# Kernel tuning notes

Measured on AMD Instinct MI355X. Metric: run time of the kernel, lower is better.

The kernel has to match this reference:

```python
import jax, jax.numpy as jnp
import numpy as np

STRIDE = 8
NUM_POINTS = 17
OFFSET_RANGE = 1.5
NUM_HEADS = 4
BASE_OFFSETS = np.array([(-1,-1),(-1,0),(-1,1),(0,-1),(0,0),(0,1),(1,-1),(1,0),(1,1),
                         (-3,-3),(-3,0),(-3,3),(0,-3),(0,3),(3,-3),(3,0),(3,3)], dtype=np.float32)


def setup_inputs() -> dict:
    key = jax.random.key(0)
    ks = jax.random.split(key, 16)
    N, D, P, B = 40000, 128, NUM_POINTS, 2
    Hf, Wf, H_img, W_img = 56, 100, 448, 800
    x_lidar = jax.random.normal(ks[0], (N, D), jnp.float32)
    b_idx = jax.random.randint(ks[1], (N, 1), 0, B)
    z = jax.random.randint(ks[2], (N, 1), 0, 10)
    y = jax.random.randint(ks[3], (N, 1), 0, 125)
    x = jax.random.randint(ks[4], (N, 1), 0, 125)
    indices = jnp.concatenate([b_idx, z, y, x], axis=1).astype(jnp.int32)
    img_feats = jax.random.normal(ks[5], (B, D, Hf, Wf), jnp.float32)
    voxel_size = jnp.array([0.1, 0.1, 0.1], jnp.float32)
    pc_range = jnp.array([-50.0, -50.0, -5.0, 50.0, 50.0, 3.0], jnp.float32)
    # plausible lidar->image projection: intrinsics @ extrinsics (x-forward -> z-forward)
    K = np.array([[600.0, 0.0, W_img / 2.0], [0.0, 600.0, H_img / 2.0], [0.0, 0.0, 1.0]])
    Rt = np.array([[0.0, -1.0, 0.0, 0.0], [0.0, 0.0, -1.0, 1.5], [1.0, 0.0, 0.0, 0.0]])
    P34 = (K @ Rt).astype(np.float32)
    trans_lidar_to_img = jnp.asarray(np.stack([P34, P34]))
    s = 0.02
    return {
        'x_lidar': x_lidar,
        'indices': indices,
        'img_feats': img_feats,
        'voxel_size': voxel_size,
        'pc_range': pc_range,
        'trans_lidar_to_img': trans_lidar_to_img,
        'offset_W': jax.random.normal(ks[6], (D, 2 * P), jnp.float32) * s,
        'offset_b': jax.random.normal(ks[7], (2 * P,), jnp.float32) * s,
        'q_W': jax.random.normal(ks[8], (D, D), jnp.float32) * s,
        'q_b': jnp.zeros((D,), jnp.float32),
        'k_W': jax.random.normal(ks[9], (D, D), jnp.float32) * s,
        'k_b': jnp.zeros((D,), jnp.float32),
        'v_W': jax.random.normal(ks[10], (D, D), jnp.float32) * s,
        'v_b': jnp.zeros((D,), jnp.float32),
        'out_W': jax.random.normal(ks[11], (D, D), jnp.float32) * s,
        'out_b': jnp.zeros((D,), jnp.float32),
        'H_img': H_img,
        'W_img': W_img,
    }


def _forward(x_lidar, indices, img_feats, voxel_size, pc_range, trans_lidar_to_img,
             offset_W, offset_b, q_W, q_b, k_W, k_b, v_W, v_b, out_W, out_b, H_img, W_img):
    N, D = x_lidar.shape
    B, C, Hf, Wf = img_feats.shape
    bidx = indices[:, 0].astype(jnp.int32)
    # --- project voxel centers to normalized image coords ---
    spatial = indices[:, jnp.array([3, 2, 1])].astype(jnp.float32)  # (x, y, z) order
    cvs = voxel_size * STRIDE
    phys = spatial * cvs + pc_range[:3] + cvs * 0.5                 # [N,3]
    hom = jnp.concatenate([phys, jnp.ones((N, 1), phys.dtype)], axis=1)
    pts = jnp.einsum('nij,nj->ni', trans_lidar_to_img[bidx], hom)   # [N,3]
    depth = jnp.maximum(pts[:, 2], 1e-5)
    u_feat = (pts[:, 0] / depth) * (float(Wf) / float(W_img))
    v_feat = (pts[:, 1] / depth) * (float(Hf) / float(H_img))
    u_n = 2.0 * (u_feat / max(Wf - 1, 1)) - 1.0
    v_n = 2.0 * (v_feat / max(Hf - 1, 1)) - 1.0
    centers = jnp.stack([u_n, v_n], axis=-1)                        # [N,2]
    # --- sampling grid: base ring + learned tanh offsets ---
    du = 2.0 / max(Wf - 1, 1)
    dv = 2.0 / max(Hf - 1, 1)
    base = jnp.asarray(BASE_OFFSETS) * jnp.array([du, dv], jnp.float32)  # [P,2]
    learned = jnp.tanh(x_lidar @ offset_W + offset_b).reshape(N, NUM_POINTS, 2)
    learned = learned * jnp.array([OFFSET_RANGE * du, OFFSET_RANGE * dv], jnp.float32)
    grid = centers[:, None, :] + base[None] + learned               # [N,P,2]
    gx, gy = grid[..., 0], grid[..., 1]
    valid = (jnp.abs(gx) <= 1.0) & (jnp.abs(gy) <= 1.0)             # [N,P]
    # --- bilinear grid_sample, align_corners=True, zeros padding, batched gather ---
    px = (gx + 1.0) * 0.5 * (Wf - 1)
    py = (gy + 1.0) * 0.5 * (Hf - 1)
    x0 = jnp.floor(px).astype(jnp.int32)
    y0 = jnp.floor(py).astype(jnp.int32)
    fx = px - x0
    fy = py - y0
    sampled = jnp.zeros((N, NUM_POINTS, C), x_lidar.dtype)
    for dx_, wx in ((0, 1.0 - fx), (1, fx)):
        for dy_, wy in ((0, 1.0 - fy), (1, fy)):
            xc = x0 + dx_
            yc = y0 + dy_
            inb = (xc >= 0) & (xc < Wf) & (yc >= 0) & (yc < Hf)
            w = wx * wy * inb
            val = img_feats[bidx[:, None], :, jnp.clip(yc, 0, Hf - 1), jnp.clip(xc, 0, Wf - 1)]  # [N,P,C]
            sampled = sampled + val * w[..., None]
    # --- single-query cross attention over sampled points ---
    scale = float(D // NUM_HEADS) ** -0.5
    q = x_lidar @ q_W + q_b                                         # [N,D]
    k = sampled @ k_W + k_b                                         # [N,P,D]
    v = sampled @ v_W + v_b
    attn = jnp.einsum('nd,npd->np', q, k) * scale
    attn = jnp.where(valid, attn, -10000.0)
    attn = jax.nn.softmax(attn, axis=-1)
    attn = attn * valid
    attn = attn / jnp.maximum(attn.sum(-1, keepdims=True), 1e-6)
    out = jnp.einsum('np,npd->nd', attn, v)
    out = out @ out_W + out_b
    # --- rectifier stats ---
    offset_scale = OFFSET_RANGE * max((du ** 2 + dv ** 2) ** 0.5, 1e-6)
    instability = jnp.linalg.norm(learned, axis=-1).mean(-1, keepdims=True) / offset_scale
    offset_stability = jnp.clip(jnp.exp(-instability), 0.0, 1.0)
    valid_sample_ratio = valid.astype(jnp.float32).mean(-1, keepdims=True)
    p = jnp.clip(attn, 1e-6, None)
    entropy = -(p * jnp.log(p)).sum(-1, keepdims=True)
    attn_focus = jnp.clip(1.0 - entropy / float(np.log(max(NUM_POINTS, 2))), 0.0, 1.0)
    return out, valid_sample_ratio, offset_stability, attn_focus


def reference(x_lidar, indices, img_feats, voxel_size, pc_range, trans_lidar_to_img,
              offset_W, offset_b, q_W, q_b, k_W, k_b, v_W, v_b, out_W, out_b, H_img, W_img):
    return _forward(x_lidar, indices, img_feats, voxel_size, pc_range, trans_lidar_to_img,
                    offset_W, offset_b, q_W, q_b, k_W, k_b, v_W, v_b, out_W, out_b, H_img, W_img)
```

## Files before the change

kernel.cpp:

```cpp
#include <hip/hip_runtime.h>
#include <hip/hip_fp16.h>
#include <math.h>

#define NPTS 17
#define DCH 128
#define HF 56
#define WF 100

using half8 = __attribute__((ext_vector_type(8))) _Float16;
using f32x4 = __attribute__((ext_vector_type(4))) float;

#define OFF_WKB    0
#define OFF_A0     128
#define OFF_B0     256
#define OFF_C0     384
#define OFF_W2T    512
#define OFF_BMT    8704
#define OFF_WOFS   16896
#define OFF_FEAT   23040
#define OFF_UVB    739840
#define OFF_IDX    899840
#define OFF_CNT    939840

__device__ inline __half2 bc_h2(unsigned u) { return __builtin_bit_cast(__half2, u); }
__device__ inline unsigned bc_u32(__half2 h) { return __builtin_bit_cast(unsigned, h); }
__device__ inline unsigned packh2(float a, float b) {
  return bc_u32(__float22half2_rn(make_float2(a, b)));
}
__device__ inline ushort f2hu(float x) {
  __half h = __float2half(x);
  return __builtin_bit_cast(ushort, h);
}

__device__ inline int swz(int row, int bcol) {
  return (row << 8) + (bcol ^ ((row & 7) << 4));
}
__device__ inline int swz7(int row, int bcol) {
  return (row << 7) + (bcol ^ ((row & 7) << 4));
}

__device__ inline void project(int4 iv, const float* voxel_size,
    const float* pc_range, const float* trans, float winv, float hinv,
    float& u_n, float& v_n, int& bidx)
{
  bidx = iv.x;
  float cv0 = voxel_size[0]*8.f, cv1 = voxel_size[1]*8.f, cv2 = voxel_size[2]*8.f;
  float ph0 = (float)iv.w*cv0 + pc_range[0] + 0.5f*cv0;
  float ph1 = (float)iv.z*cv1 + pc_range[1] + 0.5f*cv1;
  float ph2 = (float)iv.y*cv2 + pc_range[2] + 0.5f*cv2;
  const float* T = trans + bidx*12;
  float p0 = T[0]*ph0 + T[1]*ph1 + T[2]*ph2  + T[3];
  float p1 = T[4]*ph0 + T[5]*ph1 + T[6]*ph2  + T[7];
  float p2 = T[8]*ph0 + T[9]*ph1 + T[10]*ph2 + T[11];
  float depth = fmaxf(p2, 1e-5f);
  u_n = 2.f*((p0/depth)*winv/99.f) - 1.f;
  v_n = 2.f*((p1/depth)*hinv/55.f) - 1.f;
}

__global__ __launch_bounds__(256) void prep_kernel(
    const float* __restrict__ img,
    const float* __restrict__ q_W, const float* __restrict__ k_W,
    const float* __restrict__ v_W, const float* __restrict__ out_W,
    const float* __restrict__ q_b, const float* __restrict__ k_b,
    const float* __restrict__ v_b,
    const float* __restrict__ offset_W,
    const int* __restrict__ indices,
    const float* __restrict__ voxel_size, const float* __restrict__ pc_range,
    const float* __restrict__ trans,
    const int* __restrict__ HimgP, const int* __restrict__ WimgP,
    float* __restrict__ ws, int N, int nbc)
{
  __shared__ __align__(16) char smraw[32768];
  int tid = threadIdx.x;
  int bid = blockIdx.x;

  if (bid < 448) {
    float* sm = (float*)smraw;
    int by = bid >> 2, q = bid & 3;
    int b = by / HF, y = by % HF;
    const float* src = img + (size_t)b*DCH*HF*WF + (size_t)q*32*HF*WF + y*WF;
    #pragma unroll
    for (int i = 0; i < 13; ++i) {
      int flat = i*256 + tid;
      if (flat < 3200) {
        int c = flat / WF;
        int x = flat - c*WF;
        sm[c*101 + x] = src[(size_t)c*HF*WF + x];
      }
    }
    __syncthreads();
    unsigned* dst = (unsigned*)((ushort*)(ws + OFF_FEAT) + (size_t)(b*HF*WF + y*WF)*DCH);
    #pragma unroll
    for (int i = 0; i < 7; ++i) {
      int flat = i*256 + tid;
      if (flat < 1600) {
        int x = flat >> 4;
        int cp = flat & 15;
        dst[(size_t)x*64 + q*16 + cp] = packh2(sm[(2*cp)*101 + x], sm[(2*cp+1)*101 + x]);
      }
    }
    return;
  }
  bid -= 448;

  if (bid < nbc) {
    int* lc = (int*)smraw;
    int lane = tid & 63;
    unsigned long long lmlt = (1ull << lane) - 1ull;
    const float du = 2.0f/99.0f, dv = 2.0f/55.0f;
    float winv = (float)WF / (float)(WimgP[0]);
    float hinv = (float)HF / (float)(HimgP[0]);
    if (tid < 2) lc[tid] = 0;
    __syncthreads();
    int myslot[4];
    bool inA[4], skipA[4];
    #pragma unroll
    for (int j = 0; j < 4; ++j) {
      int n = bid*1024 + j*256 + tid;
      bool in = (n < N);
      bool cskip = true;
      if (in) {
        float u_n, v_n; int bx;
        project(((const int4*)indices)[n], voxel_size, pc_range, trans, winv, hinv,
                u_n, v_n, bx);
        cskip = (fabsf(u_n) > 1.001f + 4.5f*du) || (fabsf(v_n) > 1.001f + 4.5f*dv);
        if (!cskip)
          ((float4*)(ws + OFF_UVB))[n] = make_float4(u_n, v_n, (float)bx, 0.f);
      }
      inA[j] = in; skipA[j] = cskip;
      unsigned long long mv = __ballot(in && !cskip);
      unsigned long long ms = __ballot(in && cskip);
      int wv = 0, wsk = 0;
      if (lane == 0) {
        wv  = atomicAdd(&lc[0], (int)__popcll(mv));
        wsk = atomicAdd(&lc[1], (int)__popcll(ms));
      }
      wv  = __shfl(wv, 0);
      wsk = __shfl(wsk, 0);
      myslot[j] = cskip ? (wsk + (int)__popcll(ms & lmlt))
                        : (wv  + (int)__popcll(mv & lmlt));
    }
    __syncthreads();
    if (tid == 0) {
      unsigned long long pk = (unsigned long long)(unsigned)lc[0]
                            | ((unsigned long long)(unsigned)lc[1] << 32);
      unsigned long long old = atomicAdd((unsigned long long*)(ws + OFF_CNT), pk);
      lc[2] = (int)(unsigned)old;
      lc[3] = (int)(unsigned)(old >> 32);
    }
    __syncthreads();
    int* idx = (int*)(ws + OFF_IDX);
    #pragma unroll
    for (int j = 0; j < 4; ++j) {
      int n = bid*1024 + j*256 + tid;
      if (inA[j]) {
        if (!skipA[j]) idx[lc[2] + myslot[j]] = n;
        else           idx[N - 1 - (lc[3] + myslot[j])] = n;
      }
    }
    return;
  }
  bid -= nbc;

  if (bid == 0) {
    char* Als = smraw;
    char* Bls = smraw + 16384;
    ushort* w2t = (ushort*)(ws + OFF_W2T);
    int wid = tid >> 6, l = tid & 63, lr = l & 15, lg = l >> 4;
    f32x4 acc[2][8] = {};
    for (int ko = 0; ko < 2; ++ko) {
      __syncthreads();
      #pragma unroll
      for (int i = 0; i < 16; ++i) {
        int flat = i*256 + tid;
        int r = flat >> 5, kp = flat & 31;
        float2 va = *(const float2*)&k_W[r*DCH + ko*64 + 2*kp];
        float2 vb = *(const float2*)&q_W[r*DCH + ko*64 + 2*kp];
        *(unsigned*)(Als + swz7(r, kp*4)) = packh2(va.x, va.y);
        *(unsigned*)(Bls + swz7(r, kp*4)) = packh2(vb.x, vb.y);
      }
      __syncthreads();
      #pragma unroll
      for (int kc = 0; kc < 2; ++kc) {
        int kb = kc*64 + lg*16;
        half8 a0 = *(const half8*)(Als + swz7(wid*32 + lr, kb));
        half8 a1 = *(const half8*)(Als + swz7(wid*32 + 16 + lr, kb));
        #pragma unroll
        for (int ni = 0; ni < 8; ++ni) {
          half8 b = *(const half8*)(Bls + swz7(ni*16 + lr, kb));
          acc[0][ni] = __builtin_amdgcn_mfma_f32_16x16x32_f16(a0, b, acc[0][ni], 0, 0, 0);
          acc[1][ni] = __builtin_amdgcn_mfma_f32_16x16x32_f16(a1, b, acc[1][ni], 0, 0, 0);
        }
      }
    }
    #pragma unroll
    for (int mi = 0; mi < 2; ++mi)
      #pragma unroll
      for (int reg = 0; reg < 4; ++reg) {
        int n = wid*32 + mi*16 + lg*4 + reg;
        #pragma unroll
        for (int ni = 0; ni < 8; ++ni)
          w2t[n*DCH + ni*16 + lr] = f2hu(acc[mi][ni][reg]);
      }
    return;
  }
  bid -= 1;

  if (bid == 0) {
    char* Als = smraw;
    char* Bls = smraw + 16384;
    ushort* bmt = (ushort*)(ws + OFF_BMT);
    int wid = tid >> 6, l = tid & 63, lr = l & 15, lg = l >> 4;
    f32x4 acc[2][8] = {};
    for (int ko = 0; ko < 2; ++ko) {
      __syncthreads();
// ... 45 lines not shown
    __syncthreads();
    int r = tid & 127;
    const float* M  = (tid < 128) ? k_W : q_W;
    const float* vv = (tid < 128) ? vbs : vbs + 128;
    float acc = 0.f;
    #pragma unroll 8
    for (int e = 0; e < DCH; e += 4) {
      float4 m = *(const float4*)&M[(size_t)r*DCH + e];
      acc += m.x*vv[e] + m.y*vv[e+1] + m.z*vv[e+2] + m.w*vv[e+3];
    }
    ws[((tid < 128) ? OFF_A0 : OFF_WKB) + r] = acc;
    if (tid < 128) {
      float b0 = 0.f;
      #pragma unroll 8
      for (int e = 0; e < DCH; ++e) b0 += vbs[256 + e] * out_W[(size_t)e*DCH + tid];
      ws[OFF_B0 + tid] = b0;
    }
    if (tid < 64) {
      float c = vbs[tid]*vbs[128+tid] + vbs[64+tid]*vbs[192+tid];
      c += __shfl_xor(c, 32); c += __shfl_xor(c, 16); c += __shfl_xor(c, 8);
      c += __shfl_xor(c, 4);  c += __shfl_xor(c, 2);  c += __shfl_xor(c, 1);
      if (tid == 0) ws[OFF_C0] = c;
    }
    ushort* woh = (ushort*)(ws + OFF_WOFS);
    ushort* wol = woh + 48*128;
    #pragma unroll
    for (int i = 0; i < 24; ++i) {
      int flat = i*256 + tid;
      int c = flat >> 7, k = flat & 127;
      float wv = (c < 34) ? offset_W[(size_t)k*34 + c] : 0.f;
      __half hw = __float2half(wv);
      woh[flat] = __builtin_bit_cast(ushort, hw);
      wol[flat] = f2hu(wv - __half2float(hw));
    }
  }
}

__device__ inline void fill_point(float* out, const float* out_b,
                                  float instab, int pt, int mm, int N)
{
  const float du = 2.0f/99.0f, dv = 2.0f/55.0f;
  *(float4*)&out[(size_t)pt*DCH + 8*mm]     = *(const float4*)&out_b[8*mm];
  *(float4*)&out[(size_t)pt*DCH + 8*mm + 4] = *(const float4*)&out_b[8*mm + 4];
  if (mm == 0) {
    out[(size_t)N*128 + pt] = 0.f;
    float osc = 1.5f * sqrtf(du*du + dv*dv);
    float inst = (instab / 17.f) / fmaxf(osc, 1e-6f);
    out[(size_t)N*129 + pt] = fminf(fmaxf(__expf(-inst), 0.f), 1.f);
    float ent = 17.f * 1.3815511e-5f;
    out[(size_t)N*130 + pt] = fminf(fmaxf(1.f - ent / logf(17.f), 0.f), 1.f);
  }
}

__global__ __launch_bounds__(256) void fuse_kernel(
    const float* __restrict__ X,
    const float* __restrict__ offset_b,
    const float* __restrict__ out_b,
    float* __restrict__ ws, float* __restrict__ out, int N)
{
  __shared__ __align__(16) char B_lds[32768];
  __shared__ __align__(16) char A_lds[4096];
  __shared__ __align__(16) char Q_lds[4096];
  __shared__ float lrn_lds[16][36];
  __shared__ float sa_lds[16];

  int tid  = threadIdx.x;
  int wave = tid >> 6, lane = tid & 63;
  int g = lane >> 4, mm = lane & 15;
  int lr = lane & 15, lg = lane >> 4;
  int n0 = blockIdx.x * 16;
  int nvalid = ((const int*)(ws + OFF_CNT))[0];
  const int* idxp = (const int*)(ws + OFF_IDX);
  int slot = n0 + wave*4 + g;
  int row  = wave*4 + g;

  {
    int r  = tid >> 4;
    int k0 = (tid & 15) * 8;
    int sl = n0 + r; if (sl >= N) sl = N - 1;
    int pr = idxp[sl];
    const float* xp = &X[(size_t)pr*DCH + k0];
    float4 v0 = *(const float4*)xp;
    float4 v1 = *(const float4*)(xp + 4);
    __half h0 = __float2half(v0.x), h1 = __float2half(v0.y);
    __half h2 = __float2half(v0.z), h3 = __float2half(v0.w);
    __half h4 = __float2half(v1.x), h5 = __float2half(v1.y);
    __half h6 = __float2half(v1.z), h7 = __float2half(v1.w);
    uint4 hw;
    hw.x = bc_u32(__halves2half2(h0, h1)); hw.y = bc_u32(__halves2half2(h2, h3));
    hw.z = bc_u32(__halves2half2(h4, h5)); hw.w = bc_u32(__halves2half2(h6, h7));
    uint4 lw;
    lw.x = packh2(v0.x - __half2float(h0), v0.y - __half2float(h1));
    lw.y = packh2(v0.z - __half2float(h2), v0.w - __half2float(h3));
    lw.z = packh2(v1.x - __half2float(h4), v1.y - __half2float(h5));
    lw.w = packh2(v1.z - __half2float(h6), v1.w - __half2float(h7));
    *(uint4*)(A_lds + swz(r, k0*2)) = hw;
    *(uint4*)(Q_lds + swz(r, k0*2)) = lw;
  }
  {
    const ushort* woh = (const ushort*)(ws + OFF_WOFS);
    const ushort* wol = woh + 48*128;
    #pragma unroll
    for (int i = 0; i < 3; ++i) {
      int flat = i*256 + tid;
      int r = flat >> 4, kq = (flat & 15) * 8;
      *(uint4*)(B_lds + swz(r, kq*2))         = *(const uint4*)&woh[r*128 + kq];
      *(uint4*)(B_lds + 12288 + swz(r, kq*2)) = *(const uint4*)&wol[r*128 + kq];
    }
  }
  __syncthreads();

  const float du = 2.0f/99.0f, dv = 2.0f/55.0f;

  if (wave < 3) {
    f32x4 acc = {};
    #pragma unroll
    for (int kc = 0; kc < 4; ++kc) {
      int kb = kc*64 + lg*16;
      half8 ah = *(const half8*)(A_lds + swz(lr, kb));
      half8 al = *(const half8*)(Q_lds + swz(lr, kb));
      half8 bh = *(const half8*)(B_lds + swz(wave*16 + lr, kb));
      half8 bl = *(const half8*)(B_lds + 12288 + swz(wave*16 + lr, kb));
      acc = __builtin_amdgcn_mfma_f32_16x16x32_f16(al, bh, acc, 0, 0, 0);
      acc = __builtin_amdgcn_mfma_f32_16x16x32_f16(ah, bl, acc, 0, 0, 0);
      acc = __builtin_amdgcn_mfma_f32_16x16x32_f16(ah, bh, acc, 0, 0, 0);
    }
    int o = wave*16 + lr;
    if (o < 34) {
      float sc = (o & 1) ? 1.5f*dv : 1.5f*du;
      float ob = offset_b[o];
      #pragma unroll
      for (int reg = 0; reg < 4; ++reg)
        lrn_lds[lg*4 + reg][o] = tanhf(acc[reg] + ob) * sc;
    }
  }

  float ck;
  {
    uint4 xr = *(const uint4*)(A_lds + swz(row, 16*mm));
    const float* wk = ws + OFF_WKB + 8*mm;
    __half2 x01 = bc_h2(xr.x), x23 = bc_h2(xr.y), x45 = bc_h2(xr.z), x67 = bc_h2(xr.w);
    float s = __low2float(x01)*wk[0] + __high2float(x01)*wk[1]
            + __low2float(x23)*wk[2] + __high2float(x23)*wk[3]
            + __low2float(x45)*wk[4] + __high2float(x45)*wk[5]
            + __low2float(x67)*wk[6] + __high2float(x67)*wk[7];
    s += __shfl_xor(s, 8); s += __shfl_xor(s, 4);
    s += __shfl_xor(s, 2); s += __shfl_xor(s, 1);
    ck = s + ws[OFF_C0];
  }
  __syncthreads();

  float instab;
  {
    float a = lrn_lds[row][2*mm], b = lrn_lds[row][2*mm + 1];
    float s = sqrtf(a*a + b*b);
    if (mm == 0) {
      float a2 = lrn_lds[row][32], b2 = lrn_lds[row][33];
      s += sqrtf(a2*a2 + b2*b2);
    }
    s += __shfl_xor(s, 1); s += __shfl_xor(s, 2);
    s += __shfl_xor(s, 4); s += __shfl_xor(s, 8);
    instab = s;
  }

  if (n0 >= nvalid) {
    if (slot < N) fill_point(out, out_b, instab, idxp[slot], mm, N);
    return;
  }

  {
    const ushort* w2t = (const ushort*)(ws + OFF_W2T);
    #pragma unroll
    for (int i = 0; i < 8; ++i) {
      int flat = i*2048 + tid*8;
      int r = flat >> 7, k = flat & 127;
      *(uint4*)(B_lds + swz(r, k*2)) = *(const uint4*)&w2t[(size_t)r*DCH + k];
    }
  }
  __syncthreads();

  {
    f32x4 qacc[2] = {};
    #pragma unroll
    for (int kc = 0; kc < 4; ++kc) {
      int kb = kc*64 + lg*16;
      half8 a  = *(const half8*)(A_lds + swz(lr, kb));
      half8 b0 = *(const half8*)(B_lds + swz(wave*32 + lr, kb));
      half8 b1 = *(const half8*)(B_lds + swz(wave*32 + 16 + lr, kb));
      qacc[0] = __builtin_amdgcn_mfma_f32_16x16x32_f16(a, b0, qacc[0], 0, 0, 0);
      qacc[1] = __builtin_amdgcn_mfma_f32_16x16x32_f16(a, b1, qacc[1], 0, 0, 0);
    }
    #pragma unroll
    for (int ni = 0; ni < 2; ++ni)
      #pragma unroll
      for (int reg = 0; reg < 4; ++reg) {
        int r = lg*4 + reg;
        int c = wave*32 + ni*16 + lr;
        *(ushort*)(Q_lds + swz(r, c*2)) = f2hu(qacc[ni][reg] + ws[OFF_A0 + c]);
      }
  }
  __syncthreads();

  {
    const ushort* bmt = (const ushort*)(ws + OFF_BMT);
    #pragma unroll
    for (int i = 0; i < 8; ++i) {
      int flat = i*2048 + tid*8;
      int r = flat >> 7, k = flat & 127;
      *(uint4*)(B_lds + swz(r, k*2)) = *(const uint4*)&bmt[(size_t)r*DCH + k];
    }
  }

  if (slot >= nvalid) {
    if (mm == 0) sa_lds[row] = 0.f;
    uint4 z; z.x = 0u; z.y = 0u; z.z = 0u; z.w = 0u;
    *(uint4*)(Q_lds + swz(row, 16*mm)) = z;
    if (slot < N) fill_point(out, out_b, instab, idxp[slot], mm, N);
  } else {
    int pt = idxp[slot];
    float4 uv = ((const float4*)(ws + OFF_UVB))[pt];
    float u_n = uv.x, v_n = uv.y;
    int bidx = (int)uv.z;

    uint4 qp = *(const uint4*)(Q_lds + swz(row, 16*mm));
    __half2 q01 = bc_h2(qp.x), q23 = bc_h2(qp.y), q45 = bc_h2(qp.z), q67 = bc_h2(qp.w);

    const float BOX[NPTS] = {-1,-1,-1, 0,0,0, 1,1,1, -3,-3,-3, 0,0, 3,3,3};
    const float BOY[NPTS] = {-1, 0, 1,-1,0,1,-1,0,1, -3, 0, 3, -3,3,-3,0,3};
    const float scale = 0.17677669529663689f;
    const char* fb = (const char*)(ws + OFF_FEAT);

    float larr[NPTS];
    unsigned vm = 0;
    float m_run = -1e28f, srun = 0.f;
    __half2 pre01 = __float2half2_rn(0.f), pre23 = __float2half2_rn(0.f);
    __half2 pre45 = __float2half2_rn(0.f), pre67 = __float2half2_rn(0.f);
    int fbase = bidx * (HF*WF);
    int moff = mm * 16;

    #pragma unroll
    for (int p = 0; p < NPTS; ++p) {
      float2 lrn = *(const float2*)&lrn_lds[row][2*p];
      float gx = u_n + BOX[p]*du + lrn.x;
      float gy = v_n + BOY[p]*dv + lrn.y;
      bool valid = (fabsf(gx) <= 1.f) && (fabsf(gy) <= 1.f);
      float l = -1e30f;
      if (valid) {
        vm |= (1u << p);
        float px = fmaf(gx, 49.5f, 49.5f);
        float py = fmaf(gy, 27.5f, 27.5f);
        float fpx = floorf(px), fpy = floorf(py);
        float fx = px - fpx, fy = py - fpy;
        int x0 = (int)fpx, y0 = (int)fpy;
        int x1 = min(x0 + 1, WF - 1), y1 = min(y0 + 1, HF - 1);
        float wy0 = 1.f - fy, wx0 = 1.f - fx;
        __half2 h00 = __float2half2_rn(wy0*wx0);
        __half2 h01 = __float2half2_rn(wy0*fx);
        __half2 h10 = __float2half2_rn(fy*wx0);
        __half2 h11 = __float2half2_rn(fy*fx);
        int r0 = (fbase + y0*WF) << 8, r1 = (fbase + y1*WF) << 8;
        uint4 f00 = *(const uint4*)(fb + r0 + (x0 << 8) + moff);
        uint4 f01 = *(const uint4*)(fb + r0 + (x1 << 8) + moff);
        uint4 f10 = *(const uint4*)(fb + r1 + (x0 << 8) + moff);
        uint4 f11 = *(const uint4*)(fb + r1 + (x1 << 8) + moff);
        __half2 s01 = __hfma2(h00, bc_h2(f00.x),
                      __hfma2(h01, bc_h2(f01.x),
                      __hfma2(h10, bc_h2(f10.x),
                      __hmul2(h11, bc_h2(f11.x)))));
        __half2 s23 = __hfma2(h00, bc_h2(f00.y),
                      __hfma2(h01, bc_h2(f01.y),
                      __hfma2(h10, bc_h2(f10.y),
                      __hmul2(h11, bc_h2(f11.y)))));
        __half2 s45 = __hfma2(h00, bc_h2(f00.z),
                      __hfma2(h01, bc_h2(f01.z),
                      __hfma2(h10, bc_h2(f10.z),
                      __hmul2(h11, bc_h2(f11.z)))));
        __half2 s67 = __hfma2(h00, bc_h2(f00.w),
                      __hfma2(h01, bc_h2(f01.w),
                      __hfma2(h10, bc_h2(f10.w),
                      __hmul2(h11, bc_h2(f11.w)))));
        __half2 dh = __hfma2(s01, q01, __hfma2(s23, q23,
                     __hfma2(s45, q45, __hmul2(s67, q67))));
        float part = __low2float(dh) + __high2float(dh);
        part += __shfl_xor(part, 8);
        part += __shfl_xor(part, 4);
        part += __shfl_xor(part, 2);
        part += __shfl_xor(part, 1);
        l = (part + ck) * scale;
        float nm  = fmaxf(m_run, l);
        float esc = __expf(m_run - nm);
        float a   = __expf(l - nm);
        m_run = nm;
        srun = srun*esc + a;
        __half2 esch = __float2half2_rn(esc);
        __half2 ah   = __float2half2_rn(a);
        pre01 = __hfma2(ah, s01, __hmul2(pre01, esch));
        pre23 = __hfma2(ah, s23, __hmul2(pre23, esch));
        pre45 = __hfma2(ah, s45, __hmul2(pre45, esch));
        pre67 = __hfma2(ah, s67, __hmul2(pre67, esch));
      }
      larr[p] = l;
    }

    bool anyv = (vm != 0);
    float offv = anyv ? (m_run + __logf(srun)) : 1e38f;
    float invs = anyv ? 1.f/srun : 0.f;
    __half2 ih = __float2half2_rn(invs);
    pre01 = __hmul2(pre01, ih);
    pre23 = __hmul2(pre23, ih);
    pre45 = __hmul2(pre45, ih);
    pre67 = __hmul2(pre67, ih);

    float ent = 0.f;
    #pragma unroll
    for (int p = 0; p < NPTS; ++p) {
      float d = offv - larr[p];
      float a = __expf(-d);
      ent += (a >= 1e-6f) ? a*d : 1.3815511e-5f;
    }

    uint4 pw;
    pw.x = bc_u32(pre01);
    pw.y = bc_u32(pre23);
    pw.z = bc_u32(pre45);
    pw.w = bc_u32(pre67);
    *(uint4*)(Q_lds + swz(row, 16*mm)) = pw;
    if (mm == 0) {
      sa_lds[row] = anyv ? 1.f : 0.f;
      out[(size_t)N*128 + pt] = (float)__popc(vm) / 17.f;
      float osc = 1.5f * sqrtf(du*du + dv*dv);
      float inst = (instab / 17.f) / fmaxf(osc, 1e-6f);
      out[(size_t)N*129 + pt] = fminf(fmaxf(__expf(-inst), 0.f), 1.f);
      out[(size_t)N*130 + pt] = fminf(fmaxf(1.f - ent / logf(17.f), 0.f), 1.f);
    }
  }
  __syncthreads();

  {
    f32x4 oacc[2] = {};
    #pragma unroll
    for (int kc = 0; kc < 4; ++kc) {
      int kb = kc*64 + lg*16;
      half8 a  = *(const half8*)(Q_lds + swz(lr, kb));
      half8 b0 = *(const half8*)(B_lds + swz(wave*32 + lr, kb));
      half8 b1 = *(const half8*)(B_lds + swz(wave*32 + 16 + lr, kb));
      oacc[0] = __builtin_amdgcn_mfma_f32_16x16x32_f16(a, b0, oacc[0], 0, 0, 0);
      oacc[1] = __builtin_amdgcn_mfma_f32_16x16x32_f16(a, b1, oacc[1], 0, 0, 0);
    }
    #pragma unroll
    for (int reg = 0; reg < 4; ++reg) {
      int r = lg*4 + reg;
      int sl2 = n0 + r;
      if (sl2 >= nvalid) continue;
      int p2 = idxp[sl2];
      float sa = sa_lds[r];
      #pragma unroll
      for (int ni = 0; ni < 2; ++ni) {
        int c = wave*32 + ni*16 + lr;
        out[(size_t)p2*DCH + c] = oacc[ni][reg] + sa*ws[OFF_B0 + c] + out_b[c];
      }
    }
  }
}

extern "C" void kernel_launch(void* const* d_in, const int* in_sizes, int n_in,
                              void* d_out, int out_size, void* d_ws, size_t ws_size,
                              hipStream_t stream) {
  const float* x_lidar    = (const float*)d_in[0];
  const int*   indices    = (const int*)  d_in[1];
  const float* img        = (const float*)d_in[2];
  const float* voxel_size = (const float*)d_in[3];
  const float* pc_range   = (const float*)d_in[4];
  const float* trans      = (const float*)d_in[5];
  const float* offset_W   = (const float*)d_in[6];
  const float* offset_b   = (const float*)d_in[7];
  const float* q_W        = (const float*)d_in[8];
  const float* q_b        = (const float*)d_in[9];
  const float* k_W        = (const float*)d_in[10];
  const float* k_b        = (const float*)d_in[11];
  const float* v_W        = (const float*)d_in[12];
  const float* v_b        = (const float*)d_in[13];
  const float* out_W      = (const float*)d_in[14];
  const float* out_b      = (const float*)d_in[15];
  const int*   Himg       = (const int*)  d_in[16];
  const int*   Wimg       = (const int*)  d_in[17];
  float* ws  = (float*)d_ws;
  float* out = (float*)d_out;
  int N = in_sizes[0] / DCH;
  int nbc = (N + 1023) / 1024;

  hipMemsetAsync(ws + OFF_CNT, 0, 2*sizeof(int), stream);
  hipLaunchKernelGGL(prep_kernel, dim3(448 + nbc + 3), dim3(256), 0, stream,
                     img, q_W, k_W, v_W, out_W, q_b, k_b, v_b,
                     offset_W, indices, voxel_size, pc_range, trans,
                     Himg, Wimg, ws, N, nbc);
  hipLaunchKernelGGL(fuse_kernel, dim3((N + 15) / 16), dim3(256), 0, stream,
                     x_lidar, offset_b, out_b, ws, out, N);
}
```

Baseline: 47.45 us.

## Replace global atomic compaction with per-segment local compaction, drop memset

The valid/skip point compaction now happens separately in each 1024-point segment: each prep block writes its own valid count and index list into its segment region rather than reserving space through a global 64-bit atomic. The fuse kernel grid becomes 64 blocks per segment and reads its segment's count. This removes the hipMemsetAsync call, the global atomic and one block barrier. In exchange, some fuse blocks now mix valid and skipped points or exit at once, so the work per block is less uniform than with one global sorted list.

After: 63.38 us. 1.34x slower.

```diff
diff --git a/kernel.cpp b/kernel.cpp
--- a/kernel.cpp
+++ b/kernel.cpp
@@ -20,7 +20,7 @@
 #define OFF_FEAT   23040
 #define OFF_UVB    739840
 #define OFF_IDX    899840
-#define OFF_CNT    939840
+#define OFF_SCNT   939840
 
 __device__ inline __half2 bc_h2(unsigned u) { return __builtin_bit_cast(__half2, u); }
 __device__ inline unsigned bc_u32(__half2 h) { return __builtin_bit_cast(unsigned, h); }
@@ -68,7 +68,7 @@
     const float* __restrict__ voxel_size, const float* __restrict__ pc_range,
     const float* __restrict__ trans,
     const int* __restrict__ HimgP, const int* __restrict__ WimgP,
-    float* __restrict__ ws, int N, int nbc)
+    float* __restrict__ ws, int N, int nseg)
 {
   __shared__ __align__(16) char smraw[32768];
   int tid = threadIdx.x;
@@ -103,8 +103,11 @@
   }
   bid -= 448;
 
-  if (bid < nbc) {
+  if (bid < nseg) {
     int* lc = (int*)smraw;
+    int seg = bid;
+    int base = seg << 10;
+    int seg_n = N - base; if (seg_n > 1024) seg_n = 1024;
     int lane = tid & 63;
     unsigned long long lmlt = (1ull << lane) - 1ull;
     const float du = 2.0f/99.0f, dv = 2.0f/55.0f;
@@ -116,8 +119,9 @@
     bool inA[4], skipA[4];
     #pragma unroll
     for (int j = 0; j < 4; ++j) {
-      int n = bid*1024 + j*256 + tid;
-      bool in = (n < N);
+      int loc = j*256 + tid;
+      int n = base + loc;
+      bool in = (loc < seg_n);
       bool cskip = true;
       if (in) {
         float u_n, v_n; int bx;
@@ -141,26 +145,19 @@
                         : (wv  + (int)__popcll(mv & lmlt));
     }
     __syncthreads();
-    if (tid == 0) {
-      unsigned long long pk = (unsigned long long)(unsigned)lc[0]
-                            | ((unsigned long long)(unsigned)lc[1] << 32);
-      unsigned long long old = atomicAdd((unsigned long long*)(ws + OFF_CNT), pk);
-      lc[2] = (int)(unsigned)old;
-      lc[3] = (int)(unsigned)(old >> 32);
-    }
-    __syncthreads();
-    int* idx = (int*)(ws + OFF_IDX);
+    if (tid == 0) ((int*)(ws + OFF_SCNT))[seg] = lc[0];
+    int* idx = (int*)(ws + OFF_IDX) + base;
     #pragma unroll
     for (int j = 0; j < 4; ++j) {
-      int n = bid*1024 + j*256 + tid;
+      int n = base + j*256 + tid;
       if (inA[j]) {
-        if (!skipA[j]) idx[lc[2] + myslot[j]] = n;
-        else           idx[N - 1 - (lc[3] + myslot[j])] = n;
+        if (!skipA[j]) idx[myslot[j]] = n;
+        else           idx[seg_n - 1 - myslot[j]] = n;
       }
     }
     return;
   }
-  bid -= nbc;
+  bid -= nseg;
 
   if (bid == 0) {
     char* Als = smraw;
@@ -328,16 +325,21 @@
   int wave = tid >> 6, lane = tid & 63;
   int g = lane >> 4, mm = lane & 15;
   int lr = lane & 15, lg = lane >> 4;
-  int n0 = blockIdx.x * 16;
-  int nvalid = ((const int*)(ws + OFF_CNT))[0];
-  const int* idxp = (const int*)(ws + OFF_IDX);
-  int slot = n0 + wave*4 + g;
+  int seg  = blockIdx.x >> 6;
+  int jblk = blockIdx.x & 63;
+  int base = seg << 10;
+  int seg_n = N - base; if (seg_n > 1024) seg_n = 1024;
+  int n0l = jblk * 16;
+  if (n0l >= seg_n) return;
+  int nvalid = ((const int*)(ws + OFF_SCNT))[seg];
+  const int* idxp = (const int*)(ws + OFF_IDX) + base;
+  int slot = n0l + wave*4 + g;
   int row  = wave*4 + g;
 
   {
     int r  = tid >> 4;
     int k0 = (tid & 15) * 8;
-    int sl = n0 + r; if (sl >= N) sl = N - 1;
+    int sl = n0l + r; if (sl >= seg_n) sl = seg_n - 1;
     int pr = idxp[sl];
     const float* xp = &X[(size_t)pr*DCH + k0];
     float4 v0 = *(const float4*)xp;
@@ -423,8 +425,8 @@
     instab = s;
   }
 
-  if (n0 >= nvalid) {
-    if (slot < N) fill_point(out, out_b, instab, idxp[slot], mm, N);
+  if (n0l >= nvalid) {
+    if (slot < seg_n) fill_point(out, out_b, instab, idxp[slot], mm, N);
     return;
   }
 
@@ -475,7 +477,7 @@
     if (mm == 0) sa_lds[row] = 0.f;
     uint4 z; z.x = 0u; z.y = 0u; z.z = 0u; z.w = 0u;
     *(uint4*)(Q_lds + swz(row, 16*mm)) = z;
-    if (slot < N) fill_point(out, out_b, instab, idxp[slot], mm, N);
+    if (slot < seg_n) fill_point(out, out_b, instab, idxp[slot], mm, N);
   } else {
     int pt = idxp[slot];
     float4 uv = ((const float4*)(ws + OFF_UVB))[pt];
@@ -610,7 +612,7 @@
     #pragma unroll
     for (int reg = 0; reg < 4; ++reg) {
       int r = lg*4 + reg;
-      int sl2 = n0 + r;
+      int sl2 = n0l + r;
       if (sl2 >= nvalid) continue;
       int p2 = idxp[sl2];
       float sa = sa_lds[r];
@@ -647,13 +649,12 @@
   float* ws  = (float*)d_ws;
   float* out = (float*)d_out;
   int N = in_sizes[0] / DCH;
-  int nbc = (N + 1023) / 1024;
-
-  hipMemsetAsync(ws + OFF_CNT, 0, 2*sizeof(int), stream);
-  hipLaunchKernelGGL(prep_kernel, dim3(448 + nbc + 3), dim3(256), 0, stream,
+  int nseg = (N + 1023) / 1024;
+
+  hipLaunchKernelGGL(prep_kernel, dim3(448 + nseg + 3), dim3(256), 0, stream,
                      img, q_W, k_W, v_W, out_W, q_b, k_b, v_b,
                      offset_W, indices, voxel_size, pc_range, trans,
-                     Himg, Wimg, ws, N, nbc);
-  hipLaunchKernelGGL(fuse_kernel, dim3((N + 15) / 16), dim3(256), 0, stream,
+                     Himg, Wimg, ws, N, nseg);
+  hipLaunchKernelGGL(fuse_kernel, dim3(nseg * 64), dim3(256), 0, stream,
                      x_lidar, offset_b, out_b, ws, out, N);
 }
```

## Split invalid-point fill into separate 64-row kernel; early-exit heavy kernel

Applied to the files above, without the earlier changes.

Moves the output fill for points with no valid image samples out of the fused attention kernel into a dedicated fill_kernel. That kernel processes 64 rows per block, computing the offset projection with plain fp16 MFMA to get the instability statistic. The heavy kernel now exits immediately for blocks past the valid count, avoiding LDS staging and offset GEMM work for invalid points. This adds a third kernel launch and a second offset-GEMM path at lower precision for the invalid points.

New measurement: 55.11 us. 1.16x slower.

```diff
diff --git a/kernel.cpp b/kernel.cpp
--- a/kernel.cpp
+++ b/kernel.cpp
@@ -312,7 +312,96 @@
   }
 }
 
-__global__ __launch_bounds__(256) void fuse_kernel(
+__global__ __launch_bounds__(256) void fill_kernel(
+    const float* __restrict__ X,
+    const float* __restrict__ offset_b,
+    const float* __restrict__ out_b,
+    float* __restrict__ ws, float* __restrict__ out, int N)
+{
+  __shared__ __align__(16) char Ah_lds[16384];
+  __shared__ __align__(16) char Bh_lds[12288];
+  __shared__ float lrn_lds[64][36];
+
+  int tid = threadIdx.x;
+  int wave = tid >> 6, lane = tid & 63;
+  int g = lane >> 4, mm = lane & 15;
+  int lr = lane & 15, lg = lane >> 4;
+  int nvalid = ((const int*)(ws + OFF_CNT))[0];
+  int n0 = blockIdx.x * 64;
+  if (n0 + 64 <= nvalid) return;
+  const int* idxp = (const int*)(ws + OFF_IDX);
+
+  #pragma unroll
+  for (int i = 0; i < 4; ++i) {
+    int flat = i*256 + tid;
+    int r = flat >> 4, k0 = (flat & 15) * 8;
+    int sl = n0 + r; if (sl >= N) sl = N - 1;
+    int pr = idxp[sl];
+    const float* xp = &X[(size_t)pr*DCH + k0];
+    float4 v0 = *(const float4*)xp;
+    float4 v1 = *(const float4*)(xp + 4);
+    uint4 hw;
+    hw.x = packh2(v0.x, v0.y); hw.y = packh2(v0.z, v0.w);
+    hw.z = packh2(v1.x, v1.y); hw.w = packh2(v1.z, v1.w);
+    *(uint4*)(Ah_lds + swz(r, k0*2)) = hw;
+  }
+  {
+    const ushort* woh = (const ushort*)(ws + OFF_WOFS);
+    #pragma unroll
+    for (int i = 0; i < 3; ++i) {
+      int flat = i*256 + tid;
+      int r = flat >> 4, kq = (flat & 15) * 8;
+      *(uint4*)(Bh_lds + swz(r, kq*2)) = *(const uint4*)&woh[r*128 + kq];
+    }
+  }
+  __syncthreads();
+
+  const float du = 2.0f/99.0f, dv = 2.0f/55.0f;
+
+  {
+    f32x4 acc[3] = {};
+    #pragma unroll
+    for (int kc = 0; kc < 4; ++kc) {
+      int kb = kc*64 + lg*16;
+      half8 a = *(const half8*)(Ah_lds + swz(wave*16 + lr, kb));
+      #pragma unroll
+      for (int bn = 0; bn < 3; ++bn) {
+        half8 b = *(const half8*)(Bh_lds + swz(bn*16 + lr, kb));
+        acc[bn] = __builtin_amdgcn_mfma_f32_16x16x32_f16(a, b, acc[bn], 0, 0, 0);
+      }
+    }
+    #pragma unroll
+    for (int bn = 0; bn < 3; ++bn) {
+      int o = bn*16 + lr;
+      if (o < 34) {
+        float sc = (o & 1) ? 1.5f*dv : 1.5f*du;
+        float ob = offset_b[o];
+        #pragma unroll
+        for (int reg = 0; reg < 4; ++reg)
+          lrn_lds[wave*16 + lg*4 + reg][o] = tanhf(acc[bn][reg] + ob) * sc;
+      }
+    }
+  }
+  __syncthreads();
+
+  #pragma unroll
+  for (int j = 0; j < 4; ++j) {
+    int rr = wave*16 + g*4 + j;
+    int slot = n0 + rr;
+    float a = lrn_lds[rr][2*mm], b = lrn_lds[rr][2*mm + 1];
+    float s = sqrtf(a*a + b*b);
+    if (mm == 0) {
+      float a2 = lrn_lds[rr][32], b2 = lrn_lds[rr][33];
+      s += sqrtf(a2*a2 + b2*b2);
+    }
+    s += __shfl_xor(s, 1); s += __shfl_xor(s, 2);
+    s += __shfl_xor(s, 4); s += __shfl_xor(s, 8);
+    if (slot >= nvalid && slot < N)
+      fill_point(out, out_b, s, idxp[slot], mm, N);
+  }
+}
+
+__global__ __launch_bounds__(256) void heavy_kernel(
     const float* __restrict__ X,
     const float* __restrict__ offset_b,
     const float* __restrict__ out_b,
@@ -330,6 +419,7 @@
   int lr = lane & 15, lg = lane >> 4;
   int n0 = blockIdx.x * 16;
   int nvalid = ((const int*)(ws + OFF_CNT))[0];
+  if (n0 >= nvalid) return;
   const int* idxp = (const int*)(ws + OFF_IDX);
   int slot = n0 + wave*4 + g;
   int row  = wave*4 + g;
@@ -337,7 +427,7 @@
   {
     int r  = tid >> 4;
     int k0 = (tid & 15) * 8;
-    int sl = n0 + r; if (sl >= N) sl = N - 1;
+    int sl = n0 + r; if (sl >= nvalid) sl = nvalid - 1;
     int pr = idxp[sl];
     const float* xp = &X[(size_t)pr*DCH + k0];
     float4 v0 = *(const float4*)xp;
@@ -423,11 +513,6 @@
     instab = s;
   }
 
-  if (n0 >= nvalid) {
-    if (slot < N) fill_point(out, out_b, instab, idxp[slot], mm, N);
-    return;
-  }
-
   {
     const ushort* w2t = (const ushort*)(ws + OFF_W2T);
     #pragma unroll
@@ -475,7 +560,6 @@
     if (mm == 0) sa_lds[row] = 0.f;
     uint4 z; z.x = 0u; z.y = 0u; z.z = 0u; z.w = 0u;
     *(uint4*)(Q_lds + swz(row, 16*mm)) = z;
-    if (slot < N) fill_point(out, out_b, instab, idxp[slot], mm, N);
   } else {
     int pt = idxp[slot];
     float4 uv = ((const float4*)(ws + OFF_UVB))[pt];
@@ -654,6 +738,8 @@
                      img, q_W, k_W, v_W, out_W, q_b, k_b, v_b,
                      offset_W, indices, voxel_size, pc_range, trans,
                      Himg, Wimg, ws, N, nbc);
-  hipLaunchKernelGGL(fuse_kernel, dim3((N + 15) / 16), dim3(256), 0, stream,
+  hipLaunchKernelGGL(fill_kernel, dim3((N + 63) / 64), dim3(256), 0, stream,
                      x_lidar, offset_b, out_b, ws, out, N);
-}
+  hipLaunchKernelGGL(heavy_kernel, dim3((N + 15) / 16), dim3(256), 0, stream,
+                     x_lidar, offset_b, out_b, ws, out, N);
+}
```

## Split fused kernel into offset kernel and compacted heavy attention kernel

Applied to the files above, without the earlier changes.

The single fused kernel is split in two. The first kernel computes learned offsets and instability for all points in 32-row blocks and writes them to workspace, and it also fills outputs for skipped points. The second kernel runs only on compacted valid points, reloading the offsets per point, and it separates the bilinear sampling loop from the online-softmax loop so the feature loads can be issued ahead of the dependent reductions. This avoids wasted work for skipped blocks in the heavy kernel, but adds a kernel launch, extra global traffic for the offsets, and register pressure from holding the sampled values of all 17 points at once.

After: 59.20 us. +24.8%, slower.

```diff
diff --git a/kernel.cpp b/kernel.cpp
--- a/kernel.cpp
+++ b/kernel.cpp
@@ -21,6 +21,8 @@
 #define OFF_UVB    739840
 #define OFF_IDX    899840
 #define OFF_CNT    939840
+#define OFF_LRN    940032
+#define OFF_INSTAB 2300032
 
 __device__ inline __half2 bc_h2(unsigned u) { return __builtin_bit_cast(__half2, u); }
 __device__ inline unsigned bc_u32(__half2 h) { return __builtin_bit_cast(unsigned, h); }
@@ -124,8 +126,8 @@
         project(((const int4*)indices)[n], voxel_size, pc_range, trans, winv, hinv,
                 u_n, v_n, bx);
         cskip = (fabsf(u_n) > 1.001f + 4.5f*du) || (fabsf(v_n) > 1.001f + 4.5f*dv);
-        if (!cskip)
-          ((float4*)(ws + OFF_UVB))[n] = make_float4(u_n, v_n, (float)bx, 0.f);
+        ((float4*)(ws + OFF_UVB))[n] =
+            make_float4(u_n, v_n, (float)bx, cskip ? 1.f : 0.f);
       }
       inA[j] = in; skipA[j] = cskip;
       unsigned long long mv = __ballot(in && !cskip);
@@ -312,34 +314,27 @@
   }
 }
 
-__global__ __launch_bounds__(256) void fuse_kernel(
-    const float* __restrict__ X,
-    const float* __restrict__ offset_b,
+__global__ __launch_bounds__(256) void ofs_kernel(
+    const float* __restrict__ X, const float* __restrict__ offset_b,
     const float* __restrict__ out_b,
     float* __restrict__ ws, float* __restrict__ out, int N)
 {
-  __shared__ __align__(16) char B_lds[32768];
-  __shared__ __align__(16) char A_lds[4096];
-  __shared__ __align__(16) char Q_lds[4096];
-  __shared__ float lrn_lds[16][36];
-  __shared__ float sa_lds[16];
-
-  int tid  = threadIdx.x;
+  __shared__ __align__(16) char Ah[8192], Al[8192];
+  __shared__ __align__(16) char Bh[12288], Bl[12288];
+  __shared__ float lrn_lds[32][36];
+
+  int tid = threadIdx.x;
   int wave = tid >> 6, lane = tid & 63;
   int g = lane >> 4, mm = lane & 15;
   int lr = lane & 15, lg = lane >> 4;
-  int n0 = blockIdx.x * 16;
-  int nvalid = ((const int*)(ws + OFF_CNT))[0];
-  const int* idxp = (const int*)(ws + OFF_IDX);
-  int slot = n0 + wave*4 + g;
-  int row  = wave*4 + g;
-
-  {
-    int r  = tid >> 4;
-    int k0 = (tid & 15) * 8;
-    int sl = n0 + r; if (sl >= N) sl = N - 1;
-    int pr = idxp[sl];
-    const float* xp = &X[(size_t)pr*DCH + k0];
+  int n0 = blockIdx.x * 32;
+
+  #pragma unroll
+  for (int i = 0; i < 2; ++i) {
+    int flat = i*256 + tid;
+    int r = flat >> 4, k0 = (flat & 15) * 8;
+    int n = n0 + r; if (n >= N) n = N - 1;
+    const float* xp = &X[(size_t)n*DCH + k0];
     float4 v0 = *(const float4*)xp;
     float4 v1 = *(const float4*)(xp + 4);
     __half h0 = __float2half(v0.x), h1 = __float2half(v0.y);
@@ -354,8 +349,8 @@
     lw.y = packh2(v0.z - __half2float(h2), v0.w - __half2float(h3));
     lw.z = packh2(v1.x - __half2float(h4), v1.y - __half2float(h5));
     lw.w = packh2(v1.z - __half2float(h6), v1.w - __half2float(h7));
-    *(uint4*)(A_lds + swz(r, k0*2)) = hw;
-    *(uint4*)(Q_lds + swz(r, k0*2)) = lw;
+    *(uint4*)(Ah + swz(r, k0*2)) = hw;
+    *(uint4*)(Al + swz(r, k0*2)) = lw;
   }
   {
     const ushort* woh = (const ushort*)(ws + OFF_WOFS);
@@ -364,36 +359,130 @@
     for (int i = 0; i < 3; ++i) {
       int flat = i*256 + tid;
       int r = flat >> 4, kq = (flat & 15) * 8;
-      *(uint4*)(B_lds + swz(r, kq*2))         = *(const uint4*)&woh[r*128 + kq];
-      *(uint4*)(B_lds + 12288 + swz(r, kq*2)) = *(const uint4*)&wol[r*128 + kq];
+      *(uint4*)(Bh + swz(r, kq*2)) = *(const uint4*)&woh[r*128 + kq];
+      *(uint4*)(Bl + swz(r, kq*2)) = *(const uint4*)&wol[r*128 + kq];
     }
   }
   __syncthreads();
 
   const float du = 2.0f/99.0f, dv = 2.0f/55.0f;
 
-  if (wave < 3) {
+  for (int t = wave; t < 6; t += 4) {
+    int rt = (t & 1) * 16, ct = t >> 1;
     f32x4 acc = {};
     #pragma unroll
     for (int kc = 0; kc < 4; ++kc) {
       int kb = kc*64 + lg*16;
-      half8 ah = *(const half8*)(A_lds + swz(lr, kb));
-      half8 al = *(const half8*)(Q_lds + swz(lr, kb));
-      half8 bh = *(const half8*)(B_lds + swz(wave*16 + lr, kb));
-      half8 bl = *(const half8*)(B_lds + 12288 + swz(wave*16 + lr, kb));
+      half8 ah = *(const half8*)(Ah + swz(rt + lr, kb));
+      half8 al = *(const half8*)(Al + swz(rt + lr, kb));
+      half8 bh = *(const half8*)(Bh + swz(ct*16 + lr, kb));
+      half8 bl = *(const half8*)(Bl + swz(ct*16 + lr, kb));
       acc = __builtin_amdgcn_mfma_f32_16x16x32_f16(al, bh, acc, 0, 0, 0);
       acc = __builtin_amdgcn_mfma_f32_16x16x32_f16(ah, bl, acc, 0, 0, 0);
       acc = __builtin_amdgcn_mfma_f32_16x16x32_f16(ah, bh, acc, 0, 0, 0);
     }
-    int o = wave*16 + lr;
+    int o = ct*16 + lr;
     if (o < 34) {
       float sc = (o & 1) ? 1.5f*dv : 1.5f*du;
       float ob = offset_b[o];
       #pragma unroll
       for (int reg = 0; reg < 4; ++reg)
-        lrn_lds[lg*4 + reg][o] = tanhf(acc[reg] + ob) * sc;
-    }
-  }
+        lrn_lds[rt + lg*4 + reg][o] = tanhf(acc[reg] + ob) * sc;
+    }
+  }
+  __syncthreads();
+
+  {
+    float* LRN = ws + OFF_LRN;
+    #pragma unroll
+    for (int i = 0; i < 5; ++i) {
+      int flat = i*256 + tid;
+      if (flat < 1088) {
+        int r = flat / 34, o = flat - r*34;
+        int n = n0 + r;
+        if (n < N) LRN[(size_t)n*34 + o] = lrn_lds[r][o];
+      }
+    }
+  }
+
+  #pragma unroll
+  for (int j = 0; j < 2; ++j) {
+    int rr = (wave*4 + g) + 16*j;
+    int n = n0 + rr;
+    float a = lrn_lds[rr][2*mm], b = lrn_lds[rr][2*mm + 1];
+    float s = sqrtf(a*a + b*b);
+    if (mm == 0) {
+      float a2 = lrn_lds[rr][32], b2 = lrn_lds[rr][33];
+      s += sqrtf(a2*a2 + b2*b2);
+    }
+    s += __shfl_xor(s, 1); s += __shfl_xor(s, 2);
+    s += __shfl_xor(s, 4); s += __shfl_xor(s, 8);
+    if (n < N) {
+      if (mm == 0) ws[OFF_INSTAB + n] = s;
+      float4 uv = ((const float4*)(ws + OFF_UVB))[n];
+      if (uv.w != 0.f) fill_point(out, out_b, s, n, mm, N);
+    }
+  }
+}
+
+__global__ __launch_bounds__(256) void heavy_kernel(
+    const float* __restrict__ X,
+    const float* __restrict__ out_b,
+    float* __restrict__ ws, float* __restrict__ out, int N)
+{
+  __shared__ __align__(16) char W_lds[32768];
+  __shared__ __align__(16) char A_lds[4096];
+  __shared__ __align__(16) char Q_lds[4096];
+  __shared__ float lrn_lds[16][36];
+  __shared__ float sa_lds[16];
+
+  int tid  = threadIdx.x;
+  int wave = tid >> 6, lane = tid & 63;
+  int g = lane >> 4, mm = lane & 15;
+  int lr = lane & 15, lg = lane >> 4;
+  int n0 = blockIdx.x * 16;
+  int nvalid = ((const int*)(ws + OFF_CNT))[0];
+  if (n0 >= nvalid) return;
+  const int* idxp = (const int*)(ws + OFF_IDX);
+  int slot = n0 + wave*4 + g;
+  int row  = wave*4 + g;
+
+  {
+    int r  = tid >> 4;
+    int k0 = (tid & 15) * 8;
+    int sl = n0 + r; if (sl >= nvalid) sl = nvalid - 1;
+    int pr = idxp[sl];
+    const float* xp = &X[(size_t)pr*DCH + k0];
+    float4 v0 = *(const float4*)xp;
+    float4 v1 = *(const float4*)(xp + 4);
+    uint4 hw;
+    hw.x = packh2(v0.x, v0.y); hw.y = packh2(v0.z, v0.w);
+    hw.z = packh2(v1.x, v1.y); hw.w = packh2(v1.z, v1.w);
+    *(uint4*)(A_lds + swz(r, k0*2)) = hw;
+  }
+  {
+    const ushort* w2t = (const ushort*)(ws + OFF_W2T);
+    #pragma unroll
+    for (int i = 0; i < 8; ++i) {
+      int flat = i*2048 + tid*8;
+      int r = flat >> 7, k = flat & 127;
+      *(uint4*)(W_lds + swz(r, k*2)) = *(const uint4*)&w2t[(size_t)r*DCH + k];
+    }
+  }
+  {
+    const float* LRN = ws + OFF_LRN;
+    #pragma unroll
+    for (int i = 0; i < 3; ++i) {
+      int flat = i*256 + tid;
+      if (flat < 544) {
+        int r = flat / 34, o = flat - r*34;
+        int sl = n0 + r; if (sl >= nvalid) sl = nvalid - 1;
+        int pr = idxp[sl];
+        lrn_lds[r][o] = LRN[(size_t)pr*34 + o];
+      }
+    }
+  }
+  __syncthreads();
 
   float ck;
   {
@@ -408,36 +497,13 @@
     s += __shfl_xor(s, 2); s += __shfl_xor(s, 1);
     ck = s + ws[OFF_C0];
   }
-  __syncthreads();
-
-  float instab;
-  {
-    float a = lrn_lds[row][2*mm], b = lrn_lds[row][2*mm + 1];
-    float s = sqrtf(a*a + b*b);
-    if (mm == 0) {
-      float a2 = lrn_lds[row][32], b2 = lrn_lds[row][33];
-      s += sqrtf(a2*a2 + b2*b2);
-    }
-    s += __shfl_xor(s, 1); s += __shfl_xor(s, 2);
-    s += __shfl_xor(s, 4); s += __shfl_xor(s, 8);
-    instab = s;
-  }
-
-  if (n0 >= nvalid) {
-    if (slot < N) fill_point(out, out_b, instab, idxp[slot], mm, N);
-    return;
-  }
-
-  {
-    const ushort* w2t = (const ushort*)(ws + OFF_W2T);
-    #pragma unroll
-    for (int i = 0; i < 8; ++i) {
-      int flat = i*2048 + tid*8;
-      int r = flat >> 7, k = flat & 127;
-      *(uint4*)(B_lds + swz(r, k*2)) = *(const uint4*)&w2t[(size_t)r*DCH + k];
-    }
-  }
-  __syncthreads();
+
+  float u_n = 0.f, v_n = 0.f; int bidx = 0; int pt = -1;
+  if (slot < nvalid) {
+    pt = idxp[slot];
+    float4 uv = ((const float4*)(ws + OFF_UVB))[pt];
+    u_n = uv.x; v_n = uv.y; bidx = (int)uv.z;
+  }
 
   {
     f32x4 qacc[2] = {};
@@ -445,8 +511,8 @@
     for (int kc = 0; kc < 4; ++kc) {
       int kb = kc*64 + lg*16;
       half8 a  = *(const half8*)(A_lds + swz(lr, kb));
-      half8 b0 = *(const half8*)(B_lds + swz(wave*32 + lr, kb));
-      half8 b1 = *(const half8*)(B_lds + swz(wave*32 + 16 + lr, kb));
+      half8 b0 = *(const half8*)(W_lds + swz(wave*32 + lr, kb));
+      half8 b1 = *(const half8*)(W_lds + swz(wave*32 + 16 + lr, kb));
       qacc[0] = __builtin_amdgcn_mfma_f32_16x16x32_f16(a, b0, qacc[0], 0, 0, 0);
       qacc[1] = __builtin_amdgcn_mfma_f32_16x16x32_f16(a, b1, qacc[1], 0, 0, 0);
     }
@@ -467,21 +533,17 @@
     for (int i = 0; i < 8; ++i) {
       int flat = i*2048 + tid*8;
       int r = flat >> 7, k = flat & 127;
-      *(uint4*)(B_lds + swz(r, k*2)) = *(const uint4*)&bmt[(size_t)r*DCH + k];
-    }
-  }
+      *(uint4*)(W_lds + swz(r, k*2)) = *(const uint4*)&bmt[(size_t)r*DCH + k];
+    }
+  }
+
+  const float du = 2.0f/99.0f, dv = 2.0f/55.0f;
 
   if (slot >= nvalid) {
     if (mm == 0) sa_lds[row] = 0.f;
     uint4 z; z.x = 0u; z.y = 0u; z.z = 0u; z.w = 0u;
     *(uint4*)(Q_lds + swz(row, 16*mm)) = z;
-    if (slot < N) fill_point(out, out_b, instab, idxp[slot], mm, N);
   } else {
-    int pt = idxp[slot];
-    float4 uv = ((const float4*)(ws + OFF_UVB))[pt];
-    float u_n = uv.x, v_n = uv.y;
-    int bidx = (int)uv.z;
-
     uint4 qp = *(const uint4*)(Q_lds + swz(row, 16*mm));
     __half2 q01 = bc_h2(qp.x), q23 = bc_h2(qp.y), q45 = bc_h2(qp.z), q67 = bc_h2(qp.w);
 
@@ -489,22 +551,19 @@
     const float BOY[NPTS] = {-1, 0, 1,-1,0,1,-1,0,1, -3, 0, 3, -3,3,-3,0,3};
     const float scale = 0.17677669529663689f;
     const char* fb = (const char*)(ws + OFF_FEAT);
-
-    float larr[NPTS];
-    unsigned vm = 0;
-    float m_run = -1e28f, srun = 0.f;
-    __half2 pre01 = __float2half2_rn(0.f), pre23 = __float2half2_rn(0.f);
-    __half2 pre45 = __float2half2_rn(0.f), pre67 = __float2half2_rn(0.f);
     int fbase = bidx * (HF*WF);
     int moff = mm * 16;
 
+    unsigned vm = 0;
+    __half2 sA[NPTS], sB[NPTS], sC[NPTS], sD[NPTS];
     #pragma unroll
     for (int p = 0; p < NPTS; ++p) {
       float2 lrn = *(const float2*)&lrn_lds[row][2*p];
       float gx = u_n + BOX[p]*du + lrn.x;
       float gy = v_n + BOY[p]*dv + lrn.y;
       bool valid = (fabsf(gx) <= 1.f) && (fabsf(gy) <= 1.f);
-      float l = -1e30f;
+      __half2 zz = __float2half2_rn(0.f);
+      sA[p] = zz; sB[p] = zz; sC[p] = zz; sD[p] = zz;
       if (valid) {
         vm |= (1u << p);
         float px = fmaf(gx, 49.5f, 49.5f);
@@ -523,24 +582,35 @@
         uint4 f01 = *(const uint4*)(fb + r0 + (x1 << 8) + moff);
         uint4 f10 = *(const uint4*)(fb + r1 + (x0 << 8) + moff);
         uint4 f11 = *(const uint4*)(fb + r1 + (x1 << 8) + moff);
-        __half2 s01 = __hfma2(h00, bc_h2(f00.x),
-                      __hfma2(h01, bc_h2(f01.x),
-                      __hfma2(h10, bc_h2(f10.x),
-                      __hmul2(h11, bc_h2(f11.x)))));
-        __half2 s23 = __hfma2(h00, bc_h2(f00.y),
-                      __hfma2(h01, bc_h2(f01.y),
-                      __hfma2(h10, bc_h2(f10.y),
-                      __hmul2(h11, bc_h2(f11.y)))));
-        __half2 s45 = __hfma2(h00, bc_h2(f00.z),
-                      __hfma2(h01, bc_h2(f01.z),
-                      __hfma2(h10, bc_h2(f10.z),
-                      __hmul2(h11, bc_h2(f11.z)))));
-        __half2 s67 = __hfma2(h00, bc_h2(f00.w),
-                      __hfma2(h01, bc_h2(f01.w),
-                      __hfma2(h10, bc_h2(f10.w),
-                      __hmul2(h11, bc_h2(f11.w)))));
-        __half2 dh = __hfma2(s01, q01, __hfma2(s23, q23,
-                     __hfma2(s45, q45, __hmul2(s67, q67))));
+        sA[p] = __hfma2(h00, bc_h2(f00.x),
+                __hfma2(h01, bc_h2(f01.x),
+                __hfma2(h10, bc_h2(f10.x),
+                __hmul2(h11, bc_h2(f11.x)))));
+        sB[p] = __hfma2(h00, bc_h2(f00.y),
+                __hfma2(h01, bc_h2(f01.y),
+                __hfma2(h10, bc_h2(f10.y),
+                __hmul2(h11, bc_h2(f11.y)))));
+        sC[p] = __hfma2(h00, bc_h2(f00.z),
+                __hfma2(h01, bc_h2(f01.z),
+                __hfma2(h10, bc_h2(f10.z),
+                __hmul2(h11, bc_h2(f11.z)))));
+        sD[p] = __hfma2(h00, bc_h2(f00.w),
+                __hfma2(h01, bc_h2(f01.w),
+                __hfma2(h10, bc_h2(f10.w),
+                __hmul2(h11, bc_h2(f11.w)))));
+      }
+    }
+
+    float larr[NPTS];
+    float m_run = -1e28f, srun = 0.f;
+    __half2 pre01 = __float2half2_rn(0.f), pre23 = __float2half2_rn(0.f);
+    __half2 pre45 = __float2half2_rn(0.f), pre67 = __float2half2_rn(0.f);
+    #pragma unroll
+    for (int p = 0; p < NPTS; ++p) {
+      float l = -1e30f;
+      if (vm & (1u << p)) {
+        __half2 dh = __hfma2(sA[p], q01, __hfma2(sB[p], q23,
+                     __hfma2(sC[p], q45, __hmul2(sD[p], q67))));
         float part = __low2float(dh) + __high2float(dh);
         part += __shfl_xor(part, 8);
         part += __shfl_xor(part, 4);
@@ -554,10 +624,10 @@
         srun = srun*esc + a;
         __half2 esch = __float2half2_rn(esc);
         __half2 ah   = __float2half2_rn(a);
-        pre01 = __hfma2(ah, s01, __hmul2(pre01, esch));
-        pre23 = __hfma2(ah, s23, __hmul2(pre23, esch));
-        pre45 = __hfma2(ah, s45, __hmul2(pre45, esch));
-        pre67 = __hfma2(ah, s67, __hmul2(pre67, esch));
+        pre01 = __hfma2(ah, sA[p], __hmul2(pre01, esch));
+        pre23 = __hfma2(ah, sB[p], __hmul2(pre23, esch));
+        pre45 = __hfma2(ah, sC[p], __hmul2(pre45, esch));
+        pre67 = __hfma2(ah, sD[p], __hmul2(pre67, esch));
       }
       larr[p] = l;
     }
@@ -589,6 +659,7 @@
       sa_lds[row] = anyv ? 1.f : 0.f;
       out[(size_t)N*128 + pt] = (float)__popc(vm) / 17.f;
       float osc = 1.5f * sqrtf(du*du + dv*dv);
+      float instab = ws[OFF_INSTAB + pt];
       float inst = (instab / 17.f) / fmaxf(osc, 1e-6f);
       out[(size_t)N*129 + pt] = fminf(fmaxf(__expf(-inst), 0.f), 1.f);
       out[(size_t)N*130 + pt] = fminf(fmaxf(1.f - ent / logf(17.f), 0.f), 1.f);
@@ -602,8 +673,8 @@
     for (int kc = 0; kc < 4; ++kc) {
       int kb = kc*64 + lg*16;
       half8 a  = *(const half8*)(Q_lds + swz(lr, kb));
-      half8 b0 = *(const half8*)(B_lds + swz(wave*32 + lr, kb));
-      half8 b1 = *(const half8*)(B_lds + swz(wave*32 + 16 + lr, kb));
+      half8 b0 = *(const half8*)(W_lds + swz(wave*32 + lr, kb));
+      half8 b1 = *(const half8*)(W_lds + swz(wave*32 + 16 + lr, kb));
       oacc[0] = __builtin_amdgcn_mfma_f32_16x16x32_f16(a, b0, oacc[0], 0, 0, 0);
       oacc[1] = __builtin_amdgcn_mfma_f32_16x16x32_f16(a, b1, oacc[1], 0, 0, 0);
     }
@@ -654,6 +725,8 @@
                      img, q_W, k_W, v_W, out_W, q_b, k_b, v_b,
                      offset_W, indices, voxel_size, pc_range, trans,
                      Himg, Wimg, ws, N, nbc);
-  hipLaunchKernelGGL(fuse_kernel, dim3((N + 15) / 16), dim3(256), 0, stream,
+  hipLaunchKernelGGL(ofs_kernel, dim3((N + 31) / 32), dim3(256), 0, stream,
                      x_lidar, offset_b, out_b, ws, out, N);
-}
+  hipLaunchKernelGGL(heavy_kernel, dim3((N + 15) / 16), dim3(256), 0, stream,
+                     x_lidar, out_b, ws, out, N);
+}
```
